# Kernel optimization log

Hardware: AMD Instinct MI355X
Metric: run time of the kernel (lower is better)

## Reference

```python
import jax, jax.numpy as jnp
import numpy as np
import math

# SLAYER SRM-alpha neuron / simulation constants (from netParams yaml)
THETA = 10.0     # spike threshold
TAU_SR = 10.0    # PSP (srm) kernel time constant
TAU_REF = 1.0    # refractory kernel time constant
SCALE_REF = 2.0  # refractory kernel scale
TS = 1.0         # simulation timestep
POOL_GAIN = 1.1 * THETA  # SLAYER pool: sum over window scaled by 1.1*theta

# alpha kernel eps(t) = (t/tau) * exp(1 - t/tau); at lag L*Ts this equals
# (e*Ts/tau) * L * d**L with d = exp(-Ts/tau). Convolution with it is computed
# by a fused two-state linear recurrence (lax.scan over time), matching the
# fused-scan structure of the original SLAYER CUDA kernels.

def psp(x):
    """Leaky temporal integration: x [..., T] -> psp [..., T]."""
    d = math.exp(-TS / TAU_SR)
    B = math.e * TS / TAU_SR
    xt = jnp.moveaxis(x, -1, 0)  # [T, ...]
    z = jnp.zeros_like(xt[0])
    def step(carry, xn):
        p, q = carry
        q = d * (q + p)          # q_n = sum_{m<n} x[m] (n-m) d^(n-m)
        p = d * p + xn           # p_n = sum_{m<=n} x[m] d^(n-m)
        return (p, q), B * q
    _, out = jax.lax.scan(step, (z, z), xt)
    return jnp.moveaxis(out, 0, -1)


def spike(u):
    """Threshold spike generation with refractory feedback (SRM).
    u [..., T] membrane drive -> binary spikes [..., T].
    Refractory kernel: -scaleRef*theta * (t/tauRef) * exp(1 - t/tauRef).
    """
    d = math.exp(-TS / TAU_REF)
    A = -SCALE_REF * THETA * math.e * TS / TAU_REF
    ut = jnp.moveaxis(u, -1, 0)
    z = jnp.zeros_like(ut[0])
    def surr(v):
        # hard threshold forward, sigmoid surrogate gradient (straight-through)
        hard = (v >= THETA).astype(v.dtype)
        soft = jax.nn.sigmoid((v - THETA) * (4.0 / THETA))
        return soft + jax.lax.stop_gradient(hard - soft)
    def step(carry, un):
        p, q = carry
        q = d * (q + p)
        s = surr(un + A * q)  # membrane = drive + refractory response
        p = d * p + s
        return (p, q), s
    _, out = jax.lax.scan(step, (z, z), ut)
    return jnp.moveaxis(out, 0, -1)


def conv_t(x, w, pad):
    """Per-timestep 2D conv on [N,C,H,W,T]; kernel w [O,I,kh,kw]."""
    return jax.lax.conv_general_dilated(
        x, w[..., None], window_strides=(1, 1, 1),
        padding=[(pad, pad), (pad, pad), (0, 0)],
        dimension_numbers=("NCHWT", "OIHWT", "NCHWT"))


def pool2(x):
    """SLAYER 2x2 sum-pool scaled by 1.1*theta, per timestep."""
    N, C, H, W, T = x.shape
    return x.reshape(N, C, H // 2, 2, W // 2, 2, T).sum(axis=(3, 5)) * POOL_GAIN


def dense_t(x, w):
    """Dense over (C,H,W) per timestep: x [N,C,H,W,T], w [O,C,H,W] -> [N,O,T]."""
    return jnp.einsum("nchwt,ochw->not", x, w)


def setup_inputs() -> dict:
    key = jax.random.key(0)
    k0, k1, k2, k3, k4 = jax.random.split(key, 5)
    spikeInput = (jax.random.uniform(k0, (8, 1, 30, 30, 300)) < 0.05).astype(jnp.float32)
    conv1_w = jax.random.normal(k1, (16, 1, 5, 5), jnp.float32) * 1.0
    conv2_w = jax.random.normal(k2, (32, 16, 3, 3), jnp.float32) * 0.5
    conv3_w = jax.random.normal(k3, (64, 32, 3, 3), jnp.float32) * 0.5
    fc1_w = jax.random.normal(k4, (10, 64, 7, 7), jnp.float32) * 0.5
    return {"spikeInput": spikeInput, "conv1_w": conv1_w, "conv2_w": conv2_w,
            "conv3_w": conv3_w, "fc1_w": fc1_w}


def reference(spikeInput, conv1_w, conv2_w, conv3_w, fc1_w):
    s1 = spike(conv_t(psp(spikeInput), conv1_w, pad=1))  # [8,16,28,28,300]
    s2 = spike(pool2(psp(s1)))                            # [8,16,14,14,300]
    s3 = spike(conv_t(psp(s2), conv2_w, pad=1))           # [8,32,14,14,300]
    s4 = spike(pool2(psp(s3)))                            # [8,32,7,7,300]
    s5 = spike(conv_t(psp(s4), conv3_w, pad=1))           # [8,64,7,7,300]
    out = spike(dense_t(psp(s5), fc1_w))                  # [8,10,300]
    return out
```

## Files before the change

kernel.cpp:

```cpp
#include <hip/hip_runtime.h>
#include <hip/hip_bf16.h>
#include <cstdint>

#define TT 300
#define NB 8

static constexpr float D_SR  = 0.90483741803595957f;
static constexpr float B_SR  = 0.27182818284590454f;
static constexpr float D_RF  = 0.36787944117144233f;
static constexpr float A_RF  = -54.365636569180902f;
static constexpr float THETA_F = 10.0f;
static constexpr float PGAIN = 11.0f;

typedef const float __attribute__((address_space(4)))* cfp;

__global__ void k_wtr(const float* __restrict__ w1, const float* __restrict__ w2,
                      const float* __restrict__ w3, float* __restrict__ t1,
                      float* __restrict__ t2, float* __restrict__ t3) {
    int g = blockIdx.x * blockDim.x + threadIdx.x;
    if (g < 400) {
        int oc = g / 25, s = g % 25;
        t1[s * 16 + oc] = w1[g];
    } else if (g < 400 + 4608) {
        int h = g - 400, oc = h / 144, s = h % 144;
        t2[s * 32 + oc] = w2[h];
    } else if (g < 400 + 4608 + 18432) {
        int h = g - 5008, oc = h / 288, s = h % 288;
        t3[s * 64 + oc] = w3[h];
    }
}

__global__ void k_psp_tr(const float* __restrict__ in, float* __restrict__ out, int NS) {
    int i = blockIdx.x * blockDim.x + threadIdx.x;
    if (i >= NS) return;
    const float4* x4 = (const float4*)(in + (size_t)i * TT);
    constexpr int G4 = 5, NG = TT / (4 * G4);
    float4 Aa[G4], Bb[G4];
    #pragma unroll
    for (int u = 0; u < G4; ++u) Aa[u] = x4[u];
    float p = 0.f, q = 0.f;
    for (int g = 0; g < NG; ++g) {
        if (g + 1 < NG) {
            #pragma unroll
            for (int u = 0; u < G4; ++u) Bb[u] = x4[(g + 1) * G4 + u];
        }
        int t0 = g * G4 * 4;
        #pragma unroll
        for (int u = 0; u < G4; ++u) {
            float xs[4] = {Aa[u].x, Aa[u].y, Aa[u].z, Aa[u].w};
            #pragma unroll
            for (int e = 0; e < 4; ++e) {
                q = D_SR * (q + p);
                p = D_SR * p + xs[e];
                out[(size_t)(t0 + u * 4 + e) * NS + i] = B_SR * q;
            }
        }
        #pragma unroll
        for (int u = 0; u < G4; ++u) Aa[u] = Bb[u];
    }
}

template<int CI, int CO, int KS, int HI, int WI, int HO, int WO, int OCW, int J>
__global__ __launch_bounds__(256) void k_conv(const float* __restrict__ in,
                                              const float* __restrict__ wT,
                                              float* __restrict__ out) {
    constexpr int PW = WI + 2, PH = HI + 2, PST = PH * PW;
    __shared__ float lds[CI * PST];
    const int tid = threadIdx.x;
    const int tn  = blockIdx.x;
    cfp wc = (cfp)(uintptr_t)wT;
    const float* img = in + (size_t)tn * (CI * HI * WI);
    for (int idx = tid; idx < CI * PST; idx += 256) lds[idx] = 0.f;
    __syncthreads();
    for (int idx = tid; idx < CI * HI * WI; idx += 256) {
        int ic = idx / (HI * WI), rem = idx % (HI * WI);
        int r = rem / WI, c = rem % WI;
        lds[ic * PST + (r + 1) * PW + (c + 1)] = img[idx];
    }
    __syncthreads();

    const int wave = __builtin_amdgcn_readfirstlane(tid >> 6);
    const int lane = tid & 63;
    const int l = lane < 49 ? lane : 48;
    const int oc0 = (CO == OCW) ? 0 : wave * OCW;

    int pbase[J];
    #pragma unroll
    for (int j = 0; j < J; ++j) {
        int g = (CO == OCW) ? (wave * J + j) : j;
        int px = g * 49 + l;
        pbase[j] = (px / WO) * PW + (px % WO);
    }
    float acc[J * OCW];
    #pragma unroll
    for (int a = 0; a < J * OCW; ++a) acc[a] = 0.f;

    for (int ic = 0; ic < CI; ++ic) {
        #pragma unroll
        for (int kh = 0; kh < KS; ++kh) {
            #pragma unroll
            for (int kw = 0; kw < KS; ++kw) {
                const int step = (ic * KS + kh) * KS + kw;
                float iv[J];
                #pragma unroll
                for (int j = 0; j < J; ++j)
                    iv[j] = lds[ic * PST + pbase[j] + kh * PW + kw];
                #pragma unroll
                for (int o = 0; o < OCW; ++o) {
                    float wv = wc[(size_t)step * CO + oc0 + o];
                    #pragma unroll
                    for (int j = 0; j < J; ++j) acc[j * OCW + o] += iv[j] * wv;
                }
            }
        }
    }
    if (lane < 49) {
        #pragma unroll
        for (int j = 0; j < J; ++j) {
            int g = (CO == OCW) ? (wave * J + j) : j;
            int px = g * 49 + lane;
            #pragma unroll
            for (int o = 0; o < OCW; ++o)
                out[((size_t)tn * CO + oc0 + o) * (HO * WO) + px] = acc[j * OCW + o];
        }
    }
}

__global__ __launch_bounds__(256) void k_conv3(const float* __restrict__ in,
                                               const float* __restrict__ wT,
                                               float* __restrict__ out) {
    const int lane = threadIdx.x & 63;
    const int wave = __builtin_amdgcn_readfirstlane(threadIdx.x >> 6);
    const int tn   = blockIdx.x * 4 + wave;
    cfp img = (cfp)(uintptr_t)in + (size_t)tn * (32 * 49);
    const float* wp = wT + lane;
    float acc[49];
    #pragma unroll
    for (int i = 0; i < 49; ++i) acc[i] = 0.f;
    for (int ic = 0; ic < 32; ++ic) {
        float w[9];
        #pragma unroll
        for (int s = 0; s < 9; ++s) w[s] = wp[(ic * 9 + s) * 64];
        float im[49];
        #pragma unroll
        for (int k = 0; k < 49; ++k) im[k] = img[ic * 49 + k];
        #pragma unroll
        for (int kh = 0; kh < 3; ++kh) {
            #pragma unroll
            for (int kw = 0; kw < 3; ++kw) {
                #pragma unroll
                for (int r = 0; r < 7; ++r) {
                    const int ir = r + kh - 1;
                    if (ir < 0 || ir >= 7) continue;
                    #pragma unroll
                    for (int c = 0; c < 7; ++c) {
                        const int jc = c + kw - 1;
                        if (jc < 0 || jc >= 7) continue;
                        acc[r * 7 + c] += im[ir * 7 + jc] * w[kh * 3 + kw];
                    }
                }
            }
        }
    }
    #pragma unroll
    for (int px = 0; px < 49; ++px)
        out[((size_t)tn * 64 + lane) * 49 + px] = acc[px];
}

template<int C, int HI, int WI>
__global__ void k_fuse_pool(const float* __restrict__ U, float* __restrict__ X) {
    constexpr int HO = HI / 2, WO = WI / 2;
    constexpr int M   = NB * C * HO * WO;
    constexpr int NSI = NB * C * HI * WI;
    int i = blockIdx.x * blockDim.x + threadIdx.x;
    if (i >= M) return;
    int j = i % WO, r = (i / WO) % HO, nc = i / (WO * HO);
    size_t base = (size_t)(nc * HI + 2 * r) * WI + 2 * j;
    const float2* R0 = (const float2*)(U + base);
    const float2* R1 = (const float2*)(U + base + WI);
    constexpr int G = 10, NG = TT / G;
    float2 A0[G], A1[G], B0[G], B1[G];
    #pragma unroll
    for (int u = 0; u < G; ++u) {
        A0[u] = R0[(size_t)u * (NSI / 2)];
        A1[u] = R1[(size_t)u * (NSI / 2)];
    }
    float p00=0,q00=0,p01=0,q01=0,p10=0,q10=0,p11=0,q11=0;
    float P=0,Q=0, sp=0,sq=0, P2=0,Q2=0;
    for (int g = 0; g < NG; ++g) {
        if (g + 1 < NG) {
            #pragma unroll
            for (int u = 0; u < G; ++u) {
                B0[u] = R0[(size_t)((g + 1) * G + u) * (NSI / 2)];
                B1[u] = R1[(size_t)((g + 1) * G + u) * (NSI / 2)];
            }
        }
        #pragma unroll
        for (int u = 0; u < G; ++u) {
            int t = g * G + u;
            float s0, s1, s2, s3;
            q00 = D_RF*(q00+p00); { float v = A0[u].x + A_RF*q00; s0 = (v>=THETA_F)?1.f:0.f; } p00 = D_RF*p00+s0;
            q01 = D_RF*(q01+p01); { float v = A0[u].y + A_RF*q01; s1 = (v>=THETA_F)?1.f:0.f; } p01 = D_RF*p01+s1;
            q10 = D_RF*(q10+p10); { float v = A1[u].x + A_RF*q10; s2 = (v>=THETA_F)?1.f:0.f; } p10 = D_RF*p10+s2;
            q11 = D_RF*(q11+p11); { float v = A1[u].y + A_RF*q11; s3 = (v>=THETA_F)?1.f:0.f; } p11 = D_RF*p11+s3;
            float x = (s0 + s1 + s2 + s3) * PGAIN;
            Q = D_SR*(Q+P); P = D_SR*P + x; float drive = B_SR*Q;
            sq = D_RF*(sq+sp); float v2 = drive + A_RF*sq; float sv = (v2>=THETA_F)?1.f:0.f; sp = D_RF*sp+sv;
            Q2 = D_SR*(Q2+P2); P2 = D_SR*P2 + sv;
            X[(size_t)t * M + i] = B_SR * Q2;
        }
        #pragma unroll
        for (int u = 0; u < G; ++u) { A0[u] = B0[u]; A1[u] = B1[u]; }
    }
}

__global__ void k_spike_psp(const float* __restrict__ U, float* __restrict__ X, int NS) {
    int i = blockIdx.x * blockDim.x + threadIdx.x;
    if (i >= NS) return;
    constexpr int G = 20, NG = TT / G;
    float Aa[G], Bb[G];
    #pragma unroll
    for (int u = 0; u < G; ++u) Aa[u] = U[(size_t)u * NS + i];
    float p = 0, q = 0, P = 0, Q = 0;
    for (int g = 0; g < NG; ++g) {
        if (g + 1 < NG) {
            #pragma unroll
            for (int u = 0; u < G; ++u) Bb[u] = U[(size_t)((g + 1) * G + u) * NS + i];
        }
        #pragma unroll
        for (int u = 0; u < G; ++u) {
            int t = g * G + u;
            q = D_RF * (q + p);
            float v = Aa[u] + A_RF * q;
            float s = (v >= THETA_F) ? 1.f : 0.f;
            p = D_RF * p + s;
            Q = D_SR * (Q + P); P = D_SR * P + s;
            X[(size_t)t * NS + i] = B_SR * Q;
        }
        #pragma unroll
        for (int u = 0; u < G; ++u) Aa[u] = Bb[u];
    }
}

__global__ void k_dense(const float* __restrict__ X, const float* __restrict__ wf,
                        float* __restrict__ G_) {
    int tn = blockIdx.x;
    int lane = threadIdx.x;
    const float* xb = X + (size_t)tn * 3136;
    float acc[10];
    #pragma unroll
    for (int o = 0; o < 10; ++o) acc[o] = 0.f;
    for (int it = 0; it < 49; ++it) {
        int k = it * 64 + lane;
        float xv = xb[k];
        #pragma unroll
        for (int o = 0; o < 10; ++o) acc[o] += xv * wf[o * 3136 + k];
    }
    #pragma unroll
    for (int off = 32; off > 0; off >>= 1) {
        #pragma unroll
        for (int o = 0; o < 10; ++o) acc[o] += __shfl_down(acc[o], off);
    }
    if (lane == 0) {
        #pragma unroll
        for (int o = 0; o < 10; ++o) G_[tn * 10 + o] = acc[o];
    }
}

__global__ void k_spike_out(const float* __restrict__ G_, float* __restrict__ out) {
    int i = threadIdx.x;
    if (i >= 80) return;
    constexpr int G = 20, NG = TT / G;
    float Aa[G], Bb[G];
    #pragma unroll
    for (int u = 0; u < G; ++u) Aa[u] = G_[u * 80 + i];
    float p = 0, q = 0;
    for (int g = 0; g < NG; ++g) {
        if (g + 1 < NG) {
            #pragma unroll
            for (int u = 0; u < G; ++u) Bb[u] = G_[((g + 1) * G + u) * 80 + i];
        }
        #pragma unroll
        for (int u = 0; u < G; ++u) {
            int t = g * G + u;
            q = D_RF * (q + p);
            float v = Aa[u] + A_RF * q;
            float s = (v >= THETA_F) ? 1.f : 0.f;
            p = D_RF * p + s;
            out[(size_t)i * TT + t] = s;
        }
        #pragma unroll
        for (int u = 0; u < G; ++u) Aa[u] = Bb[u];
    }
}

static inline int cdiv(int a, int b) { return (a + b - 1) / b; }

extern "C" void kernel_launch(void* const* d_in, const int* in_sizes, int n_in,
                              void* d_out, int out_size, void* d_ws, size_t ws_size,
                              hipStream_t stream) {
    const float* x  = (const float*)d_in[0];
    const float* w1 = (const float*)d_in[1];
    const float* w2 = (const float*)d_in[2];
    const float* w3 = (const float*)d_in[3];
    const float* wf = (const float*)d_in[4];
    float* out = (float*)d_out;
    float* ws  = (float*)d_ws;

    float* A   = ws;
    float* U1  = ws + 2160000;
    float* X2  = ws + 32265600;
    float* Gg  = ws + 39792000;
    float* wT1 = ws + 39816000;
    float* wT2 = ws + 39816400;
    float* wT3 = ws + 39821008;
    float* U2  = U1;
    float* X4  = U1 + 16000000;
    float* U3  = X2;
    float* X5  = U1;

    const int B = 256;
    k_wtr<<<cdiv(23440, B), B, 0, stream>>>(w1, w2, w3, wT1, wT2, wT3);
    k_psp_tr<<<cdiv(7200, B), B, 0, stream>>>(x, A, 7200);
    k_conv<1, 16, 5, 30, 30, 28, 28, 16, 4><<<2400, B, 0, stream>>>(A, wT1, U1);
    k_fuse_pool<16, 28, 28><<<cdiv(25088, B), B, 0, stream>>>(U1, X2);
    k_conv<16, 32, 3, 14, 14, 14, 14, 32, 1><<<2400, B, 0, stream>>>(X2, wT2, U2);
    k_fuse_pool<32, 14, 14><<<cdiv(12544, B), B, 0, stream>>>(U2, X4);
    k_conv3<<<600, B, 0, stream>>>(X4, wT3, U3);
    k_spike_psp<<<cdiv(25088, B), B, 0, stream>>>(U3, X5, 25088);
    k_dense<<<2400, 64, 0, stream>>>(X5, wf, Gg);
    k_spike_out<<<1, 128, 0, stream>>>(Gg, out);
}
```

Before: 385.6 us.

## Split conv3 output rows across two waves and stage input image in LDS

The conv3 kernel now runs one block of two waves per (t,n) image instead of four images per 256-thread block. Each image is first staged into shared memory. Each wave then computes a subset of the output rows (0-3 or 4-6), reading input rows from LDS one at a time. This lowers per-thread accumulator registers from 49 to at most 28 and doubles the number of waves, which should raise occupancy. The cost is a shared-memory staging step, a barrier, and some input rows loaded by both waves.

```diff
diff --git a/kernel.cpp b/kernel.cpp
--- a/kernel.cpp
+++ b/kernel.cpp
@@ -126,45 +126,58 @@
     }
 }
 
-__global__ __launch_bounds__(256) void k_conv3(const float* __restrict__ in,
-                                               const float* __restrict__ wT,
-                                               float* __restrict__ out) {
-    const int lane = threadIdx.x & 63;
-    const int wave = __builtin_amdgcn_readfirstlane(threadIdx.x >> 6);
-    const int tn   = blockIdx.x * 4 + wave;
-    cfp img = (cfp)(uintptr_t)in + (size_t)tn * (32 * 49);
-    const float* wp = wT + lane;
-    float acc[49];
-    #pragma unroll
-    for (int i = 0; i < 49; ++i) acc[i] = 0.f;
+template<int RB, int RE, int IRB, int IRE>
+__device__ __forceinline__ void conv3_rows(const float* lds, const float* wp,
+                                           float* __restrict__ out, int tn, int lane) {
+    constexpr int NR = RE - RB;
+    float acc[NR * 7];
+    #pragma unroll
+    for (int a = 0; a < NR * 7; ++a) acc[a] = 0.f;
     for (int ic = 0; ic < 32; ++ic) {
         float w[9];
         #pragma unroll
         for (int s = 0; s < 9; ++s) w[s] = wp[(ic * 9 + s) * 64];
-        float im[49];
-        #pragma unroll
-        for (int k = 0; k < 49; ++k) im[k] = img[ic * 49 + k];
-        #pragma unroll
-        for (int kh = 0; kh < 3; ++kh) {
-            #pragma unroll
-            for (int kw = 0; kw < 3; ++kw) {
+        #pragma unroll
+        for (int ir = IRB; ir < IRE; ++ir) {
+            float row[7];
+            #pragma unroll
+            for (int c = 0; c < 7; ++c) row[c] = lds[ic * 49 + ir * 7 + c];
+            #pragma unroll
+            for (int kh = 0; kh < 3; ++kh) {
+                const int r = ir + 1 - kh;
+                if (r < RB || r >= RE) continue;
                 #pragma unroll
-                for (int r = 0; r < 7; ++r) {
-                    const int ir = r + kh - 1;
-                    if (ir < 0 || ir >= 7) continue;
+                for (int c = 0; c < 7; ++c) {
                     #pragma unroll
-                    for (int c = 0; c < 7; ++c) {
+                    for (int kw = 0; kw < 3; ++kw) {
                         const int jc = c + kw - 1;
                         if (jc < 0 || jc >= 7) continue;
-                        acc[r * 7 + c] += im[ir * 7 + jc] * w[kh * 3 + kw];
+                        acc[(r - RB) * 7 + c] += row[jc] * w[kh * 3 + kw];
                     }
                 }
             }
         }
     }
     #pragma unroll
-    for (int px = 0; px < 49; ++px)
-        out[((size_t)tn * 64 + lane) * 49 + px] = acc[px];
+    for (int r = RB; r < RE; ++r)
+        #pragma unroll
+        for (int c = 0; c < 7; ++c)
+            out[((size_t)tn * 64 + lane) * 49 + r * 7 + c] = acc[(r - RB) * 7 + c];
+}
+
+__global__ __launch_bounds__(128) void k_conv3(const float* __restrict__ in,
+                                               const float* __restrict__ wT,
+                                               float* __restrict__ out) {
+    __shared__ float lds[1568];
+    const int tid = threadIdx.x;
+    const int tn  = blockIdx.x;
+    const float4* src = (const float4*)(in + (size_t)tn * 1568);
+    for (int idx = tid; idx < 392; idx += 128) ((float4*)lds)[idx] = src[idx];
+    __syncthreads();
+    const int lane = tid & 63;
+    const float* wp = wT + lane;
+    if (tid < 64) conv3_rows<0, 4, 0, 5>(lds, wp, out, tn, lane);
+    else          conv3_rows<4, 7, 3, 7>(lds, wp, out, tn, lane);
 }
 
 template<int C, int HI, int WI>
@@ -326,7 +339,7 @@
     k_fuse_pool<16, 28, 28><<<cdiv(25088, B), B, 0, stream>>>(U1, X2);
     k_conv<16, 32, 3, 14, 14, 14, 14, 32, 1><<<2400, B, 0, stream>>>(X2, wT2, U2);
     k_fuse_pool<32, 14, 14><<<cdiv(12544, B), B, 0, stream>>>(U2, X4);
-    k_conv3<<<600, B, 0, stream>>>(X4, wT3, U3);
+    k_conv3<<<2400, 128, 0, stream>>>(X4, wT3, U3);
     k_spike_psp<<<cdiv(25088, B), B, 0, stream>>>(U3, X5, 25088);
     k_dense<<<2400, 64, 0, stream>>>(X5, wf, Gg);
     k_spike_out<<<1, 128, 0, stream>>>(Gg, out);
```

After: 381.5 us. No clear change (-1.1%).
